# Kernel optimization log

Measured on AMD Instinct MI355X. Metric: run time of the kernel, lower is better.

## Reference

```python
import jax, jax.numpy as jnp
import numpy as np

N_NODES = 50000
N_EDGES = 800000
NODE_DIM = 128
HIDDEN = 256
LATENT = 128
COND = 5


def setup_inputs() -> dict:
    key = jax.random.key(0)
    ks = jax.random.split(key, 10)
    s = lambda d: 1.0 / np.sqrt(d)
    return {
        "node_features": jax.random.normal(ks[0], (N_NODES, NODE_DIM), jnp.float32),
        "conditions": jax.random.normal(ks[1], (COND,), jnp.float32),
        "src": jax.random.randint(ks[2], (N_EDGES,), 0, N_NODES, jnp.int32),
        "dst": jax.random.randint(ks[3], (N_EDGES,), 0, N_NODES, jnp.int32),
        "W1": jax.random.normal(ks[4], (NODE_DIM, HIDDEN), jnp.float32) * s(NODE_DIM),
        "b1": jnp.zeros((HIDDEN,), jnp.float32),
        "W2": jax.random.normal(ks[5], (HIDDEN, HIDDEN), jnp.float32) * s(HIDDEN),
        "b2": jnp.zeros((HIDDEN,), jnp.float32),
        "Wfc": jax.random.normal(ks[6], (HIDDEN + COND, LATENT), jnp.float32) * s(HIDDEN + COND),
        "bfc": jnp.zeros((LATENT,), jnp.float32),
        "Wmean": jax.random.normal(ks[7], (LATENT, LATENT), jnp.float32) * s(LATENT),
        "bmean": jnp.zeros((LATENT,), jnp.float32),
        "Wlogvar": jax.random.normal(ks[8], (LATENT, LATENT), jnp.float32) * s(LATENT),
        "blogvar": jnp.zeros((LATENT,), jnp.float32),
    }


def _graph_conv(x, src, dst, W, b, n_nodes):
    # gather source-node features along edges, sum-aggregate onto targets,
    # then linear transform: standard GraphConv (sum aggregation)
    agg = jax.ops.segment_sum(x[src], dst, num_segments=n_nodes)  # [N, d]
    return agg @ W + b


def reference(node_features, conditions, src, dst,
              W1, b1, W2, b2, Wfc, bfc, Wmean, bmean, Wlogvar, blogvar):
    n = node_features.shape[0]
    x = jax.nn.relu(_graph_conv(node_features, src, dst, W1, b1, n))  # [N, H]
    x = jax.nn.relu(_graph_conv(x, src, dst, W2, b2, n))              # [N, H]
    pooled = jnp.mean(x, axis=0)                                      # [H]
    h = jax.nn.relu(jnp.concatenate([pooled, conditions], axis=-1) @ Wfc + bfc)
    z_mean = h @ Wmean + bmean
    z_logvar = h @ Wlogvar + blogvar
    return z_mean, z_logvar
```

## Files before the change

### kernel.cpp

```cpp
#include <hip/hip_runtime.h>

#define N_NODES   50000
#define N_EDGES   800000
#define NODE_DIM  128
#define HIDDEN    256
#define LATENT    128
#define COND      5

#define NB        196
#define P1_CHUNK  4096
#define P1_GRID   ((N_EDGES + P1_CHUNK - 1) / P1_CHUNK)

typedef unsigned int uint;
typedef unsigned short ushort;
typedef unsigned char uchar;

typedef __attribute__((ext_vector_type(8))) short bf16x8;
typedef __attribute__((ext_vector_type(4))) float f32x4;

static __device__ __forceinline__ ushort f32_to_bf16(float f) {
    union { float f; uint u; } v; v.f = f;
    uint r = v.u + 0x7FFF + ((v.u >> 16) & 1);
    return (ushort)(r >> 16);
}
static __device__ __forceinline__ uint pack_bf16(float lo, float hi) {
    return (uint)f32_to_bf16(lo) | ((uint)f32_to_bf16(hi) << 16);
}

static __device__ __forceinline__ void gload_lds16(const void* g, void* l) {
    __builtin_amdgcn_global_load_lds(
        (const __attribute__((address_space(1))) unsigned int*)(unsigned long long)(uintptr_t)g,
        (__attribute__((address_space(3))) unsigned int*)(unsigned int)(uintptr_t)l,
        16, 0, 0);
}


#if __has_builtin(__builtin_amdgcn_cvt_pk_f32_fp8) && __has_builtin(__builtin_amdgcn_cvt_pk_fp8_f32)
#define HW_FP8 1
#endif

#ifndef HW_FP8
static __device__ __forceinline__ float dec1_fp8(uint b) {
    uint sgn = b & 0x80, mag = b & 0x7f;
    float v;
    if (mag >= 8) {
        union { uint u; float f; } t;
        t.u = (((mag >> 3) + 120) << 23) | ((mag & 7) << 20);
        v = t.f;
    } else {
        v = (float)mag * 0.001953125f;
    }
    return sgn ? -v : v;
}
static __device__ __forceinline__ uchar enc1_fp8(float f) {
    float a = fabsf(f);
    uint s = (f < 0.f) ? 0x80u : 0u;
    if (!(a >= 0.015625f)) {
        int q = (int)(a * 512.f + 0.5f);
        if (q > 7) q = 7;
        return (uchar)(s | (uint)q);
    }
    if (a >= 448.f) return (uchar)(s | 0x7E);
    union { float f; uint u; } t; t.f = a;
    uint e = (t.u >> 23) - 120;
    uint m = (t.u >> 20) & 7;
    uint rem = t.u & 0xFFFFF;
    uint v = (e << 3) | m;
    if (rem > 0x80000 || (rem == 0x80000 && (v & 1))) v++;
    if (v > 0x7E) v = 0x7E;
    return (uchar)(s | v);
}
#endif

static __device__ __forceinline__ void dec4_add(uint u, float* acc) {
#ifdef HW_FP8
    auto lo = __builtin_amdgcn_cvt_pk_f32_fp8((int)u, false);
    auto hi = __builtin_amdgcn_cvt_pk_f32_fp8((int)u, true);
    acc[0] += lo[0]; acc[1] += lo[1]; acc[2] += hi[0]; acc[3] += hi[1];
#else
    acc[0] += dec1_fp8(u & 0xff);
    acc[1] += dec1_fp8((u >> 8) & 0xff);
    acc[2] += dec1_fp8((u >> 16) & 0xff);
    acc[3] += dec1_fp8(u >> 24);
#endif
}
static __device__ __forceinline__ void dec2_add(uint u, float* acc) {
#ifdef HW_FP8
    auto lo = __builtin_amdgcn_cvt_pk_f32_fp8((int)u, false);
    acc[0] += lo[0]; acc[1] += lo[1];
#else
    acc[0] += dec1_fp8(u & 0xff);
    acc[1] += dec1_fp8((u >> 8) & 0xff);
#endif
}
static __device__ __forceinline__ uint enc2_fp8(float a, float b) {
#ifdef HW_FP8
    return (uint)__builtin_amdgcn_cvt_pk_fp8_f32(a, b, 0, false) & 0xFFFFu;
#else
    return (uint)enc1_fp8(a) | ((uint)enc1_fp8(b) << 8);
#endif
}
static __device__ __forceinline__ uchar enc1(float v) {
#ifdef HW_FP8
    return (uchar)(__builtin_amdgcn_cvt_pk_fp8_f32(v, v, 0, false) & 0xff);
#else
    return enc1_fp8(v);
#endif
}


#define NF4   (N_NODES * NODE_DIM / 4)
#define PREP1 (NF4 + NODE_DIM * HIDDEN)
#define PREP2 (PREP1 + HIDDEN * HIDDEN)
#define PREP3 (PREP2 + HIDDEN)
#define PREP4 (PREP3 + NB)
#define PREP5 (PREP4 + NB)
#define PREP6 (PREP5 + 1)

__global__ void prep_kernel(const float* __restrict__ nf,
                            const float* __restrict__ W1, const float* __restrict__ W2,
                            uchar* __restrict__ nf_fp8,
                            ushort* __restrict__ Wst1, ushort* __restrict__ Wst2,
                            float* __restrict__ pooled,
                            int* __restrict__ bcount, int* __restrict__ bcursor2,
                            int* __restrict__ hcnt) {
    int id = blockIdx.x * blockDim.x + threadIdx.x;
    if (id < NF4) {
        float4 v = reinterpret_cast<const float4*>(nf)[id];
        uint w = enc2_fp8(v.x, v.y) | (enc2_fp8(v.z, v.w) << 16);
        reinterpret_cast<uint*>(nf_fp8)[id] = w;
    } else if (id < PREP1) {
        int i = id - NF4;
        int k = i >> 8, c = i & 255;
        int idx = ((((k >> 5) * 16) + (((k & 31) >> 3) * 4 + (c >> 6))) * 64 + (c & 63)) * 8 + (k & 7);
        Wst1[idx] = f32_to_bf16(W1[i]);
    } else if (id < PREP2) {
        int i = id - PREP1;
        int k = i >> 8, c = i & 255;
        int idx = ((((k >> 5) * 16) + (((k & 31) >> 3) * 4 + (c >> 6))) * 64 + (c & 63)) * 8 + (k & 7);
        Wst2[idx] = f32_to_bf16(W2[i]);
    } else if (id < PREP3) {
        pooled[id - PREP2] = 0.f;
    } else if (id < PREP4) {
        bcount[id - PREP3] = 0;
    } else if (id < PREP5) {
        bcursor2[id - PREP4] = 0;
    } else if (id < PREP6) {
        hcnt[0] = 0;
    }
}


__global__ __launch_bounds__(256) void bcount_kernel(const int* __restrict__ dst,
                                                     int* __restrict__ bcount) {
    __shared__ int cnt[NB];
    const int t = threadIdx.x;
    for (int i = t; i < NB; i += 256) cnt[i] = 0;
    __syncthreads();
    const int base = blockIdx.x * P1_CHUNK;
#pragma unroll
    for (int i = 0; i < 16; ++i) {
        int e = base + i * 256 + t;
        if (e < N_EDGES) atomicAdd(&cnt[dst[e] >> 8], 1);
    }
    __syncthreads();
    for (int i = t; i < NB; i += 256)
        if (cnt[i] > 0) atomicAdd(&bcount[i], cnt[i]);
}

__global__ __launch_bounds__(256) void bwrite_kernel(const int* __restrict__ src,
                                                     const int* __restrict__ dst,
                                                     const int* __restrict__ bcount,
                                                     int* __restrict__ bcursor2,
                                                     uint* __restrict__ pair_buf) {
    __shared__ int s[256];
    __shared__ int cnt[NB];
    __shared__ int gbase[NB];
    const int t = threadIdx.x;
    s[t] = (t < NB) ? bcount[t] : 0;
    __syncthreads();
    for (int off = 1; off < 256; off <<= 1) {
        int v = (t >= off) ? s[t - off] : 0;
        __syncthreads();
        s[t] += v;
        __syncthreads();
    }
    for (int i = t; i < NB; i += 256) cnt[i] = 0;
    __syncthreads();

    const int base = blockIdx.x * P1_CHUNK;
    uint pk[16];
    int  bk[16], lr[16];
    bool ok[16];
#pragma unroll
    for (int i = 0; i < 16; ++i) {
        int e = base + i * 256 + t;
        ok[i] = e < N_EDGES;
        if (ok[i]) {
            int sv = src[e], d = dst[e];
            pk[i] = (uint)sv | ((uint)d << 16);
            bk[i] = d >> 8;
        }
    }
#pragma unroll
    for (int i = 0; i < 16; ++i)
        if (ok[i]) lr[i] = atomicAdd(&cnt[bk[i]], 1);
    __syncthreads();
    if (t < NB) {
        int c = cnt[t];
        if (c > 0) gbase[t] = ((t > 0) ? s[t - 1] : 0) + atomicAdd(&bcursor2[t], c);
    }
    __syncthreads();
#pragma unroll
    for (int i = 0; i < 16; ++i)
        if (ok[i]) pair_buf[gbase[bk[i]] + lr[i]] = pk[i];
}

__global__ __launch_bounds__(256) void csrloc_kernel(const uint* __restrict__ pair_buf,
                                                     const int* __restrict__ bcount,
                                                     int* __restrict__ offsets,
                                                     ushort* __restrict__ csr) {
    __shared__ int s[256];
    __shared__ int lcnt[256];
    __shared__ int loff[256];
    __shared__ int lcur[256];
    const int t = threadIdx.x;
    const int b = blockIdx.x;
    s[t] = (t < NB) ? bcount[t] : 0;
    __syncthreads();
    for (int off = 1; off < 256; off <<= 1) {
        int v = (t >= off) ? s[t - off] : 0;
        __syncthreads();
        s[t] += v;
        __syncthreads();
    }
    const int e0 = (b > 0) ? s[b - 1] : 0;
    const int e1 = s[b];
    lcnt[t] = 0;
    lcur[t] = 0;
    __syncthreads();

    for (int j = e0 + t; j < e1; j += 256)
        atomicAdd(&lcnt[(pair_buf[j] >> 16) & 255], 1);
    __syncthreads();

    const int myc = lcnt[t];
    s[t] = myc;
    __syncthreads();
    for (int off = 1; off < 256; off <<= 1) {
        int v = (t >= off) ? s[t - off] : 0;
        __syncthreads();
        s[t] += v;
        __syncthreads();
    }
    const int lofft = s[t] - myc;
    loff[t] = lofft;
    const int node = (b << 8) + t;
    if (node < N_NODES) offsets[node] = e0 + lofft;
    if (b == 0 && t == 0) offsets[N_NODES] = N_EDGES;
    __syncthreads();

    for (int j = e0 + t; j < e1; j += 256) {
        uint p = pair_buf[j];
        int dl = (int)(p >> 16) & 255;
        int r = atomicAdd(&lcur[dl], 1);
        csr[e0 + loff[dl] + r] = (ushort)(p & 0xFFFFu);
    }
}


template <int D>
__global__ __launch_bounds__(256) void agg_kernel(const uchar* __restrict__ x,
                                                  const int* __restrict__ offsets,
                                                  const ushort* __restrict__ csr,
                                                  ushort* __restrict__ out) {
    constexpr int BPL = D / 64;
    int node = (blockIdx.x * blockDim.x + threadIdx.x) >> 6;
    int lane = threadIdx.x & 63;
    if (node >= N_NODES) return;
    int j0 = __builtin_amdgcn_readfirstlane(offsets[node]);
    int j1 = __builtin_amdgcn_readfirstlane(offsets[node + 1]);

    float acc[BPL];
#pragma unroll
    for (int i = 0; i < BPL; ++i) acc[i] = 0.f;

    const uchar* base = x + lane * BPL;
    const int il = lane & 15;

    int idxv = (j0 + il < j1) ? (int)csr[j0 + il] : 0;

    for (int jb = j0; jb < j1; jb += 16) {
        int idxn = (jb + 16 + il < j1) ? (int)csr[jb + 16 + il] : 0;
        int n = j1 - jb; n = (n > 16) ? 16 : n;
        uint u[16];
        if (n == 16) {
#pragma unroll
            for (int i = 0; i < 16; ++i) {
                int s = __shfl(idxv, i);
                if constexpr (BPL == 4)
                    u[i] = *reinterpret_cast<const uint*>(base + (size_t)s * D);
                else
                    u[i] = *reinterpret_cast<const ushort*>(base + (size_t)s * D);
            }
#pragma unroll
            for (int i = 0; i < 16; ++i) {
                if constexpr (BPL == 4) dec4_add(u[i], acc); else dec2_add(u[i], acc);
            }
        } else {
#pragma unroll
            for (int i = 0; i < 16; ++i) {
                if (i < n) {
                    int s = __shfl(idxv, i);
                    if constexpr (BPL == 4)
                        u[i] = *reinterpret_cast<const uint*>(base + (size_t)s * D);
                    else
                        u[i] = *reinterpret_cast<const ushort*>(base + (size_t)s * D);
                }
            }
#pragma unroll
            for (int i = 0; i < 16; ++i) {
                if (i < n) {
                    if constexpr (BPL == 4) dec4_add(u[i], acc); else dec2_add(u[i], acc);
                }
            }
        }
        idxv = idxn;
    }

    if constexpr (BPL == 4) {
        uint2 o;
        o.x = pack_bf16(acc[0], acc[1]);
        o.y = pack_bf16(acc[2], acc[3]);
        *reinterpret_cast<uint2*>(out + (size_t)node * D + lane * 4) = o;
    } else {
        *reinterpret_cast<uint*>(out + (size_t)node * D + lane * 2) = pack_bf16(acc[0], acc[1]);
    }
}


__global__ __launch_bounds__(256) void gemm1_kernel(const ushort* __restrict__ A,
                                                    const ushort* __restrict__ Wst,
                                                    const float* __restrict__ bias,
                                                    uchar* __restrict__ Xout, int nblk) {
    constexpr int K = NODE_DIM;
    constexpr int NSTEP = K / 32;
    constexpr int WB    = NSTEP * 8 * 1024;
    constexpr int AB    = NSTEP * 4 * 1024;
    constexpr int NT    = (N_NODES + 63) / 64;
    __shared__ uchar lds[WB + 2 * AB];

    const int t    = threadIdx.x;
    const int lane = t & 63;
    const int wv   = t >> 6;
    const int fr   = lane & 15;
    const int kgl  = lane >> 4;
    const int half    = nblk >> 1;
    const int colhalf = blockIdx.x / half;
    const int stride  = half;

    const int kx = (lane & 3) ^ ((lane >> 3) & 3);

#pragma unroll
    for (int j = 0; j < NSTEP * 2; ++j) {
        const int lc = wv * (NSTEP * 2) + j;
        const int ks = lc >> 3, r = lc & 7;
        const int kg = r >> 1, ccl = r & 1;
        gload_lds16(Wst + ((size_t)ks * 16 + kg * 4 + colhalf * 2 + ccl) * 512 + lane * 8,
                    &lds[lc * 1024]);
    }

    auto stageA = [&](int buf, int row0) {
#pragma unroll
        for (int j = 0; j < NSTEP; ++j) {
            const int c  = wv * NSTEP + j;
            const int ks = c >> 2, rt = c & 3;
            gload_lds16(A + (size_t)(row0 + rt * 16 + (lane >> 2)) * K + ks * 32 + kx * 8,
                        &lds[WB + buf * AB + c * 1024]);
        }
    };

    const int rowsel = (wv & 1) * 2;
    const int colsel = wv >> 1;
    const int col0   = colhalf * 128 + colsel * 64;
    float bcol[4];
#pragma unroll
    for (int ct = 0; ct < 4; ++ct) bcol[ct] = bias[col0 + ct * 16 + fr];
    const int mrow = kgl * 4;
    const int aswz = (kgl ^ ((fr >> 1) & 3)) * 16;

    int tile = blockIdx.x % half;
    stageA(0, tile * 64);
    __syncthreads();

    for (int buf = 0; tile < NT; tile += stride, buf ^= 1) {
        const int tn = tile + stride;
        if (tn < NT) stageA(buf ^ 1, tn * 64);

        f32x4 acc[2][4];
#pragma unroll
        for (int rt = 0; rt < 2; ++rt)
#pragma unroll
            for (int ct = 0; ct < 4; ++ct)
                acc[rt][ct] = (f32x4){0.f, 0.f, 0.f, 0.f};

        const uchar* ab = &lds[WB + buf * AB];
#pragma unroll
        for (int ks = 0; ks < NSTEP; ++ks) {
            bf16x8 af[2], bfv[4];
#pragma unroll
            for (int rt = 0; rt < 2; ++rt)
                af[rt] = *reinterpret_cast<const bf16x8*>(ab + (ks * 4 + rowsel + rt) * 1024 + fr * 64 + aswz);
#pragma unroll
            for (int ct = 0; ct < 4; ++ct)
                bfv[ct] = *reinterpret_cast<const bf16x8*>(&lds[(ks * 8 + kgl * 2 + colsel) * 1024 + (ct * 16 + fr) * 16]);
#pragma unroll
            for (int rt = 0; rt < 2; ++rt)
#pragma unroll
                for (int ct = 0; ct < 4; ++ct)
                    acc[rt][ct] = __builtin_amdgcn_mfma_f32_16x16x32_bf16(af[rt], bfv[ct], acc[rt][ct], 0, 0, 0);
        }

        const int rowbase = tile * 64 + (wv & 1) * 32;
#pragma unroll
        for (int rt = 0; rt < 2; ++rt) {
#pragma unroll
            for (int e = 0; e < 4; ++e) {
                int m = rowbase + rt * 16 + mrow + e;
                if (m < N_NODES) {
#pragma unroll
                    for (int ct = 0; ct < 4; ++ct) {
                        float v = fmaxf(acc[rt][ct][e] + bcol[ct], 0.f);
                        Xout[(size_t)m * HIDDEN + col0 + ct * 16 + fr] = enc1(v);
                    }
                }
            }
        }
        __syncthreads();
    }
}


__global__ __launch_bounds__(256) void gemm2_kernel(const ushort* __restrict__ A,
                                                    const ushort* __restrict__ Wst,
                                                    const float* __restrict__ bias,
                                                    float* __restrict__ pooled, int nblk,
                                                    const float* __restrict__ cond,
                                                    const float* __restrict__ Wfc,
                                                    const float* __restrict__ bfc,
                                                    const float* __restrict__ Wmean,
                                                    const float* __restrict__ bmean,
                                                    const float* __restrict__ Wlogvar,
                                                    const float* __restrict__ blogvar,
                                                    float* __restrict__ outv,
                                                    int* __restrict__ hcnt) {
    constexpr int K   = HIDDEN;
    constexpr int WB  = 32768;
    constexpr int AB  = 16384;
    constexpr int NT  = (N_NODES + 31) / 32;
    __shared__ uchar lds[WB + 2 * AB];
    __shared__ int lastflag;

    const int t    = threadIdx.x;
    const int lane = t & 63;
    const int wv   = t >> 6;
    const int fr   = lane & 15;
    const int kgl  = lane >> 4;
    const int q      = nblk >> 2;
    const int colq   = blockIdx.x / q;
    const int stride = q;

    const int kx = (lane & 3) ^ ((lane >> 3) & 3);

#pragma unroll
    for (int j = 0; j < 8; ++j) {
        const int lc = wv * 8 + j;
        const int ks = lc >> 2, kg = lc & 3;
        gload_lds16(Wst + ((size_t)ks * 16 + kg * 4 + colq) * 512 + lane * 8,
                    &lds[lc * 1024]);
    }

    auto stageA = [&](int buf, int row0) {
#pragma unroll
        for (int j = 0; j < 4; ++j) {
            const int c  = wv * 4 + j;
            const int ks = c >> 1, rh = c & 1;
            gload_lds16(A + (size_t)(row0 + rh * 16 + (lane >> 2)) * K + ks * 32 + kx * 8,
                        &lds[WB + buf * AB + c * 1024]);
        }
    };

    const int rowhalf = wv & 1;
    const int colh32  = wv >> 1;
    const int col0    = colq * 64 + colh32 * 32;
    float bcol[2];
#pragma unroll
    for (int ct = 0; ct < 2; ++ct) bcol[ct] = bias[col0 + ct * 16 + fr];
    const int mrow = kgl * 4;
    const int aswz = (kgl ^ ((fr >> 1) & 3)) * 16;

    float cs[2] = {0.f, 0.f};
    int tile = blockIdx.x % q;
    stageA(0, tile * 32);
    __syncthreads();

    for (int buf = 0; tile < NT; tile += stride, buf ^= 1) {
        const int tn = tile + stride;
        if (tn < NT) stageA(buf ^ 1, tn * 32);

        f32x4 acc[2];
        acc[0] = (f32x4){0.f, 0.f, 0.f, 0.f};
        acc[1] = (f32x4){0.f, 0.f, 0.f, 0.f};

        const uchar* ab = &lds[WB + buf * AB];
#pragma unroll
        for (int ks = 0; ks < 8; ++ks) {
            bf16x8 af, bfv[2];
            af = *reinterpret_cast<const bf16x8*>(ab + (ks * 2 + rowhalf) * 1024 + fr * 64 + aswz);
#pragma unroll
            for (int ct = 0; ct < 2; ++ct)
                bfv[ct] = *reinterpret_cast<const bf16x8*>(
                    &lds[(ks * 4 + kgl) * 1024 + (colh32 * 32 + ct * 16 + fr) * 16]);
#pragma unroll
            for (int ct = 0; ct < 2; ++ct)
                acc[ct] = __builtin_amdgcn_mfma_f32_16x16x32_bf16(af, bfv[ct], acc[ct], 0, 0, 0);
        }

        const int rowbase = tile * 32 + rowhalf * 16;
#pragma unroll
        for (int e = 0; e < 4; ++e) {
            int m = rowbase + mrow + e;
            if (m < N_NODES) {
                cs[0] += fmaxf(acc[0][e] + bcol[0], 0.f);
                cs[1] += fmaxf(acc[1][e] + bcol[1], 0.f);
            }
        }
        __syncthreads();
    }

#pragma unroll
    for (int ct = 0; ct < 2; ++ct) {
        cs[ct] += __shfl_xor(cs[ct], 16);
        cs[ct] += __shfl_xor(cs[ct], 32);
    }
    if (lane < 16) {
#pragma unroll
        for (int ct = 0; ct < 2; ++ct)
            atomicAdd(&pooled[col0 + ct * 16 + lane], cs[ct]);
    }

    asm volatile("s_waitcnt vmcnt(0)" ::: "memory");
    __syncthreads();
    if (t == 0) lastflag = (atomicAdd(hcnt, 1) == nblk - 1) ? 1 : 0;
    __syncthreads();
    if (lastflag) {
        float* hv = (float*)lds;
        float* hh = (float*)(lds + 2048);
        if (t < HIDDEN) hv[t] = atomicAdd(&pooled[t], 0.0f) * (1.0f / N_NODES);
        if (t < COND) hv[HIDDEN + t] = cond[t];
        __syncthreads();
        if (t < LATENT) {
            float s = bfc[t];
            for (int k = 0; k < HIDDEN + COND; ++k) s += hv[k] * Wfc[k * LATENT + t];
            hh[t] = fmaxf(s, 0.f);
        }
        __syncthreads();
        if (t < LATENT) {
            float s = bmean[t];
            for (int k = 0; k < LATENT; ++k) s += hh[k] * Wmean[k * LATENT + t];
            outv[t] = s;
        } else if (t < 2 * LATENT) {
            int j = t - LATENT;
            float s = blogvar[j];
            for (int k = 0; k < LATENT; ++k) s += hh[k] * Wlogvar[k * LATENT + j];
            outv[LATENT + j] = s;
        }
    }
}


extern "C" void kernel_launch(void* const* d_in, const int* in_sizes, int n_in,
                              void* d_out, int out_size, void* d_ws, size_t ws_size,
                              hipStream_t stream) {
    const float* node_features = (const float*)d_in[0];
    const float* conditions    = (const float*)d_in[1];
    const int*   src           = (const int*)d_in[2];
    const int*   dst           = (const int*)d_in[3];
    const float* W1  = (const float*)d_in[4];
    const float* b1  = (const float*)d_in[5];
    const float* W2  = (const float*)d_in[6];
    const float* b2  = (const float*)d_in[7];
    const float* Wfc = (const float*)d_in[8];
    const float* bfc = (const float*)d_in[9];
    const float* Wmean   = (const float*)d_in[10];
    const float* bmean   = (const float*)d_in[11];
    const float* Wlogvar = (const float*)d_in[12];
    const float* blogvar = (const float*)d_in[13];
    float* out = (float*)d_out;

    size_t o = 0;
    auto alloc = [&](size_t bytes) {
        void* p = (char*)d_ws + o;
        o += (bytes + 255) & ~(size_t)255;
        return p;
    };
    int* offsets   = (int*)alloc((size_t)(N_NODES + 1) * 4);
    int* bcount    = (int*)alloc((size_t)NB * 4);
    int* bcursor2  = (int*)alloc((size_t)NB * 4);
    int* hcnt      = (int*)alloc(4);
    uint* pair_buf = (uint*)alloc((size_t)N_EDGES * 4);
    ushort* csr    = (ushort*)alloc((size_t)N_EDGES * 2);
    float* pooled  = (float*)alloc(HIDDEN * 4);
    ushort* Wst1   = (ushort*)alloc((size_t)HIDDEN * NODE_DIM * 2);
    ushort* Wst2   = (ushort*)alloc((size_t)HIDDEN * HIDDEN * 2);
    uchar* nf_fp8  = (uchar*)alloc((size_t)N_NODES * NODE_DIM);
    uchar* x1_fp8  = (uchar*)alloc((size_t)N_NODES * HIDDEN);
    ushort* agg1   = (ushort*)alloc((size_t)(N_NODES + 64) * NODE_DIM * 2);
    ushort* agg2   = (ushort*)alloc((size_t)(N_NODES + 64) * HIDDEN * 2);

    prep_kernel<<<(PREP6 + 255) / 256, 256, 0, stream>>>(
        node_features, W1, W2, nf_fp8, Wst1, Wst2, pooled, bcount, bcursor2, hcnt);

    bcount_kernel<<<P1_GRID, 256, 0, stream>>>(dst, bcount);
    bwrite_kernel<<<P1_GRID, 256, 0, stream>>>(src, dst, bcount, bcursor2, pair_buf);
    csrloc_kernel<<<NB, 256, 0, stream>>>(pair_buf, bcount, offsets, csr);

    const int AGG_GRID = (N_NODES * 64 + 255) / 256;
    const int G1_BLK = 512;
    const int G2_BLK = 512;

    agg_kernel<NODE_DIM><<<AGG_GRID, 256, 0, stream>>>(nf_fp8, offsets, csr, agg1);
    gemm1_kernel<<<G1_BLK, 256, 0, stream>>>(agg1, Wst1, b1, x1_fp8, G1_BLK);

    agg_kernel<HIDDEN><<<AGG_GRID, 256, 0, stream>>>(x1_fp8, offsets, csr, agg2);
    gemm2_kernel<<<G2_BLK, 256, 0, stream>>>(
        agg2, Wst2, b2, pooled, G2_BLK,
        conditions, Wfc, bfc, Wmean, bmean, Wlogvar, blogvar, out, hcnt);
}
```

Baseline: 141.2 us.

## Load GEMM operands directly into registers instead of staging through LDS

Both GEMM kernels drop the LDS double-buffered staging with global_load_lds and instead load weight fragments once into registers and A fragments per tile directly from global memory. The weight pre-layout becomes a plain transpose (column-major bf16), and barriers inside the tile loop are removed. This is meant to cut LDS traffic and synchronisation overhead, but it loses explicit prefetch overlap and raises register pressure (launch_bounds 256,2 added), with less coalesced global reads of A.

```diff
diff --git a/kernel.cpp b/kernel.cpp
--- a/kernel.cpp
+++ b/kernel.cpp
@@ -25,13 +25,6 @@
 }
 static __device__ __forceinline__ uint pack_bf16(float lo, float hi) {
     return (uint)f32_to_bf16(lo) | ((uint)f32_to_bf16(hi) << 16);
-}
-
-static __device__ __forceinline__ void gload_lds16(const void* g, void* l) {
-    __builtin_amdgcn_global_load_lds(
-        (const __attribute__((address_space(1))) unsigned int*)(unsigned long long)(uintptr_t)g,
-        (__attribute__((address_space(3))) unsigned int*)(unsigned int)(uintptr_t)l,
-        16, 0, 0);
 }
 
 
@@ -120,7 +113,7 @@
 __global__ void prep_kernel(const float* __restrict__ nf,
                             const float* __restrict__ W1, const float* __restrict__ W2,
                             uchar* __restrict__ nf_fp8,
-                            ushort* __restrict__ Wst1, ushort* __restrict__ Wst2,
+                            ushort* __restrict__ Wt1, ushort* __restrict__ Wt2,
                             float* __restrict__ pooled,
                             int* __restrict__ bcount, int* __restrict__ bcursor2,
                             int* __restrict__ hcnt) {
@@ -132,13 +125,11 @@
     } else if (id < PREP1) {
         int i = id - NF4;
         int k = i >> 8, c = i & 255;
-        int idx = ((((k >> 5) * 16) + (((k & 31) >> 3) * 4 + (c >> 6))) * 64 + (c & 63)) * 8 + (k & 7);
-        Wst1[idx] = f32_to_bf16(W1[i]);
+        Wt1[c * NODE_DIM + k] = f32_to_bf16(W1[i]);
     } else if (id < PREP2) {
         int i = id - PREP1;
         int k = i >> 8, c = i & 255;
-        int idx = ((((k >> 5) * 16) + (((k & 31) >> 3) * 4 + (c >> 6))) * 64 + (c & 63)) * 8 + (k & 7);
-        Wst2[idx] = f32_to_bf16(W2[i]);
+        Wt2[c * HIDDEN + k] = f32_to_bf16(W2[i]);
     } else if (id < PREP3) {
         pooled[id - PREP2] = 0.f;
     } else if (id < PREP4) {
@@ -339,63 +330,48 @@
 }
 
 
-__global__ __launch_bounds__(256) void gemm1_kernel(const ushort* __restrict__ A,
-                                                    const ushort* __restrict__ Wst,
-                                                    const float* __restrict__ bias,
-                                                    uchar* __restrict__ Xout, int nblk) {
-    constexpr int K = NODE_DIM;
-    constexpr int NSTEP = K / 32;
-    constexpr int WB    = NSTEP * 8 * 1024;
-    constexpr int AB    = NSTEP * 4 * 1024;
-    constexpr int NT    = (N_NODES + 63) / 64;
-    __shared__ uchar lds[WB + 2 * AB];
-
-    const int t    = threadIdx.x;
-    const int lane = t & 63;
-    const int wv   = t >> 6;
+__global__ __launch_bounds__(256, 2) void gemm1_kernel(const ushort* __restrict__ A,
+                                                       const ushort* __restrict__ Wt,
+                                                       const float* __restrict__ bias,
+                                                       uchar* __restrict__ Xout, int nblk) {
+    constexpr int K  = NODE_DIM;
+    constexpr int NT = (N_NODES + 63) / 64;
+
+    const int lane = threadIdx.x & 63;
+    const int wv   = threadIdx.x >> 6;
     const int fr   = lane & 15;
     const int kgl  = lane >> 4;
     const int half    = nblk >> 1;
     const int colhalf = blockIdx.x / half;
     const int stride  = half;
 
-    const int kx = (lane & 3) ^ ((lane >> 3) & 3);
-
-#pragma unroll
-    for (int j = 0; j < NSTEP * 2; ++j) {
-        const int lc = wv * (NSTEP * 2) + j;
-        const int ks = lc >> 3, r = lc & 7;
-        const int kg = r >> 1, ccl = r & 1;
-        gload_lds16(Wst + ((size_t)ks * 16 + kg * 4 + colhalf * 2 + ccl) * 512 + lane * 8,
-                    &lds[lc * 1024]);
-    }
-
-    auto stageA = [&](int buf, int row0) {
-#pragma unroll
-        for (int j = 0; j < NSTEP; ++j) {
-            const int c  = wv * NSTEP + j;
-            const int ks = c >> 2, rt = c & 3;
-            gload_lds16(A + (size_t)(row0 + rt * 16 + (lane >> 2)) * K + ks * 32 + kx * 8,
-                        &lds[WB + buf * AB + c * 1024]);
-        }
-    };
-
-    const int rowsel = (wv & 1) * 2;
+    const int rowsel = (wv & 1) * 32;
     const int colsel = wv >> 1;
     const int col0   = colhalf * 128 + colsel * 64;
+
+    bf16x8 w[4][4];
+#pragma unroll
+    for (int ks = 0; ks < 4; ++ks)
+#pragma unroll
+        for (int ct = 0; ct < 4; ++ct)
+            w[ks][ct] = *reinterpret_cast<const bf16x8*>(
+                Wt + (size_t)(col0 + ct * 16 + fr) * K + ks * 32 + kgl * 8);
+
     float bcol[4];
 #pragma unroll
     for (int ct = 0; ct < 4; ++ct) bcol[ct] = bias[col0 + ct * 16 + fr];
     const int mrow = kgl * 4;
-    const int aswz = (kgl ^ ((fr >> 1) & 3)) * 16;
-
-    int tile = blockIdx.x % half;
-    stageA(0, tile * 64);
-    __syncthreads();
-
-    for (int buf = 0; tile < NT; tile += stride, buf ^= 1) {
-        const int tn = tile + stride;
-        if (tn < NT) stageA(buf ^ 1, tn * 64);
+
+    for (int tile = blockIdx.x % half; tile < NT; tile += stride) {
+        const int rowb = tile * 64 + rowsel;
+        bf16x8 af[2][4];
+#pragma unroll
+        for (int rt = 0; rt < 2; ++rt) {
+            const ushort* ap = A + (size_t)(rowb + rt * 16 + fr) * K + kgl * 8;
+#pragma unroll
+            for (int ks = 0; ks < 4; ++ks)
+                af[rt][ks] = *reinterpret_cast<const bf16x8*>(ap + ks * 32);
+        }
 
         f32x4 acc[2][4];
 #pragma unroll
@@ -404,29 +380,19 @@
             for (int ct = 0; ct < 4; ++ct)
                 acc[rt][ct] = (f32x4){0.f, 0.f, 0.f, 0.f};
 
-        const uchar* ab = &lds[WB + buf * AB];
-#pragma unroll
-        for (int ks = 0; ks < NSTEP; ++ks) {
-            bf16x8 af[2], bfv[4];
+#pragma unroll
+        for (int ks = 0; ks < 4; ++ks)
 #pragma unroll
             for (int rt = 0; rt < 2; ++rt)
-                af[rt] = *reinterpret_cast<const bf16x8*>(ab + (ks * 4 + rowsel + rt) * 1024 + fr * 64 + aswz);
-#pragma unroll
-            for (int ct = 0; ct < 4; ++ct)
-                bfv[ct] = *reinterpret_cast<const bf16x8*>(&lds[(ks * 8 + kgl * 2 + colsel) * 1024 + (ct * 16 + fr) * 16]);
-#pragma unroll
-            for (int rt = 0; rt < 2; ++rt)
 #pragma unroll
                 for (int ct = 0; ct < 4; ++ct)
-                    acc[rt][ct] = __builtin_amdgcn_mfma_f32_16x16x32_bf16(af[rt], bfv[ct], acc[rt][ct], 0, 0, 0);
-        }
-
-        const int rowbase = tile * 64 + (wv & 1) * 32;
+                    acc[rt][ct] = __builtin_amdgcn_mfma_f32_16x16x32_bf16(af[rt][ks], w[ks][ct], acc[rt][ct], 0, 0, 0);
+
 #pragma unroll
         for (int rt = 0; rt < 2; ++rt) {
 #pragma unroll
             for (int e = 0; e < 4; ++e) {
-                int m = rowbase + rt * 16 + mrow + e;
+                int m = rowb + rt * 16 + mrow + e;
                 if (m < N_NODES) {
 #pragma unroll
                     for (int ct = 0; ct < 4; ++ct) {
@@ -436,29 +402,27 @@
                 }
             }
         }
-        __syncthreads();
-    }
-}
-
-
-__global__ __launch_bounds__(256) void gemm2_kernel(const ushort* __restrict__ A,
-                                                    const ushort* __restrict__ Wst,
-                                                    const float* __restrict__ bias,
-                                                    float* __restrict__ pooled, int nblk,
-                                                    const float* __restrict__ cond,
-                                                    const float* __restrict__ Wfc,
-                                                    const float* __restrict__ bfc,
-                                                    const float* __restrict__ Wmean,
-                                                    const float* __restrict__ bmean,
-                                                    const float* __restrict__ Wlogvar,
-                                                    const float* __restrict__ blogvar,
-                                                    float* __restrict__ outv,
-                                                    int* __restrict__ hcnt) {
-    constexpr int K   = HIDDEN;
-    constexpr int WB  = 32768;
-    constexpr int AB  = 16384;
-    constexpr int NT  = (N_NODES + 31) / 32;
-    __shared__ uchar lds[WB + 2 * AB];
+    }
+}
+
+
+__global__ __launch_bounds__(256, 2) void gemm2_kernel(const ushort* __restrict__ A,
+                                                       const ushort* __restrict__ Wt,
+                                                       const float* __restrict__ bias,
+                                                       float* __restrict__ pooled, int nblk,
+                                                       const float* __restrict__ cond,
+                                                       const float* __restrict__ Wfc,
+                                                       const float* __restrict__ bfc,
+                                                       const float* __restrict__ Wmean,
+                                                       const float* __restrict__ bmean,
+                                                       const float* __restrict__ Wlogvar,
+                                                       const float* __restrict__ blogvar,
+                                                       float* __restrict__ outv,
+                                                       int* __restrict__ hcnt) {
+    constexpr int K  = HIDDEN;
+    constexpr int NT = (N_NODES + 31) / 32;
+    __shared__ float hv[HIDDEN + COND];
+    __shared__ float hh[LATENT];
     __shared__ int lastflag;
 
     const int t    = threadIdx.x;
@@ -470,72 +434,50 @@
     const int colq   = blockIdx.x / q;
     const int stride = q;
 
-    const int kx = (lane & 3) ^ ((lane >> 3) & 3);
-
-#pragma unroll
-    for (int j = 0; j < 8; ++j) {
-        const int lc = wv * 8 + j;
-        const int ks = lc >> 2, kg = lc & 3;
-        gload_lds16(Wst + ((size_t)ks * 16 + kg * 4 + colq) * 512 + lane * 8,
-                    &lds[lc * 1024]);
-    }
-
-    auto stageA = [&](int buf, int row0) {
-#pragma unroll
-        for (int j = 0; j < 4; ++j) {
-            const int c  = wv * 4 + j;
-            const int ks = c >> 1, rh = c & 1;
-            gload_lds16(A + (size_t)(row0 + rh * 16 + (lane >> 2)) * K + ks * 32 + kx * 8,
-                        &lds[WB + buf * AB + c * 1024]);
-        }
-    };
-
     const int rowhalf = wv & 1;
     const int colh32  = wv >> 1;
     const int col0    = colq * 64 + colh32 * 32;
+
+    bf16x8 w[8][2];
+#pragma unroll
+    for (int ks = 0; ks < 8; ++ks)
+#pragma unroll
+        for (int ct = 0; ct < 2; ++ct)
+            w[ks][ct] = *reinterpret_cast<const bf16x8*>(
+                Wt + (size_t)(col0 + ct * 16 + fr) * K + ks * 32 + kgl * 8);
+
     float bcol[2];
-#pragma unroll
-    for (int ct = 0; ct < 2; ++ct) bcol[ct] = bias[col0 + ct * 16 + fr];
+    bcol[0] = bias[col0 + fr];
+    bcol[1] = bias[col0 + 16 + fr];
     const int mrow = kgl * 4;
-    const int aswz = (kgl ^ ((fr >> 1) & 3)) * 16;
 
     float cs[2] = {0.f, 0.f};
-    int tile = blockIdx.x % q;
-    stageA(0, tile * 32);
-    __syncthreads();
-
-    for (int buf = 0; tile < NT; tile += stride, buf ^= 1) {
-        const int tn = tile + stride;
-        if (tn < NT) stageA(buf ^ 1, tn * 32);
+
+    for (int tile = blockIdx.x % q; tile < NT; tile += stride) {
+        const int rowb = tile * 32 + rowhalf * 16;
+        const ushort* ap = A + (size_t)(rowb + fr) * K + kgl * 8;
+        bf16x8 af[8];
+#pragma unroll
+        for (int ks = 0; ks < 8; ++ks)
+            af[ks] = *reinterpret_cast<const bf16x8*>(ap + ks * 32);
 
         f32x4 acc[2];
         acc[0] = (f32x4){0.f, 0.f, 0.f, 0.f};
         acc[1] = (f32x4){0.f, 0.f, 0.f, 0.f};
-
-        const uchar* ab = &lds[WB + buf * AB];
 #pragma unroll
         for (int ks = 0; ks < 8; ++ks) {
-            bf16x8 af, bfv[2];
-            af = *reinterpret_cast<const bf16x8*>(ab + (ks * 2 + rowhalf) * 1024 + fr * 64 + aswz);
-#pragma unroll
-            for (int ct = 0; ct < 2; ++ct)
-                bfv[ct] = *reinterpret_cast<const bf16x8*>(
-                    &lds[(ks * 4 + kgl) * 1024 + (colh32 * 32 + ct * 16 + fr) * 16]);
-#pragma unroll
-            for (int ct = 0; ct < 2; ++ct)
-                acc[ct] = __builtin_amdgcn_mfma_f32_16x16x32_bf16(af, bfv[ct], acc[ct], 0, 0, 0);
-        }
-
-        const int rowbase = tile * 32 + rowhalf * 16;
+            acc[0] = __builtin_amdgcn_mfma_f32_16x16x32_bf16(af[ks], w[ks][0], acc[0], 0, 0, 0);
+            acc[1] = __builtin_amdgcn_mfma_f32_16x16x32_bf16(af[ks], w[ks][1], acc[1], 0, 0, 0);
+        }
+
 #pragma unroll
         for (int e = 0; e < 4; ++e) {
-            int m = rowbase + mrow + e;
+            int m = rowb + mrow + e;
             if (m < N_NODES) {
                 cs[0] += fmaxf(acc[0][e] + bcol[0], 0.f);
                 cs[1] += fmaxf(acc[1][e] + bcol[1], 0.f);
             }
         }
-        __syncthreads();
     }
 
 #pragma unroll
@@ -554,8 +496,6 @@
     if (t == 0) lastflag = (atomicAdd(hcnt, 1) == nblk - 1) ? 1 : 0;
     __syncthreads();
     if (lastflag) {
-        float* hv = (float*)lds;
-        float* hh = (float*)(lds + 2048);
         if (t < HIDDEN) hv[t] = atomicAdd(&pooled[t], 0.0f) * (1.0f / N_NODES);
         if (t < COND) hv[HIDDEN + t] = cond[t];
         __syncthreads();
@@ -611,15 +551,15 @@
     uint* pair_buf = (uint*)alloc((size_t)N_EDGES * 4);
     ushort* csr    = (ushort*)alloc((size_t)N_EDGES * 2);
     float* pooled  = (float*)alloc(HIDDEN * 4);
-    ushort* Wst1   = (ushort*)alloc((size_t)HIDDEN * NODE_DIM * 2);
-    ushort* Wst2   = (ushort*)alloc((size_t)HIDDEN * HIDDEN * 2);
+    ushort* Wt1    = (ushort*)alloc((size_t)HIDDEN * NODE_DIM * 2);
+    ushort* Wt2    = (ushort*)alloc((size_t)HIDDEN * HIDDEN * 2);
     uchar* nf_fp8  = (uchar*)alloc((size_t)N_NODES * NODE_DIM);
     uchar* x1_fp8  = (uchar*)alloc((size_t)N_NODES * HIDDEN);
     ushort* agg1   = (ushort*)alloc((size_t)(N_NODES + 64) * NODE_DIM * 2);
     ushort* agg2   = (ushort*)alloc((size_t)(N_NODES + 64) * HIDDEN * 2);
 
     prep_kernel<<<(PREP6 + 255) / 256, 256, 0, stream>>>(
-        node_features, W1, W2, nf_fp8, Wst1, Wst2, pooled, bcount, bcursor2, hcnt);
+        node_features, W1, W2, nf_fp8, Wt1, Wt2, pooled, bcount, bcursor2, hcnt);
 
     bcount_kernel<<<P1_GRID, 256, 0, stream>>>(dst, bcount);
     bwrite_kernel<<<P1_GRID, 256, 0, stream>>>(src, dst, bcount, bcursor2, pair_buf);
@@ -630,10 +570,10 @@
     const int G2_BLK = 512;
 
     agg_kernel<NODE_DIM><<<AGG_GRID, 256, 0, stream>>>(nf_fp8, offsets, csr, agg1);
-    gemm1_kernel<<<G1_BLK, 256, 0, stream>>>(agg1, Wst1, b1, x1_fp8, G1_BLK);
+    gemm1_kernel<<<G1_BLK, 256, 0, stream>>>(agg1, Wt1, b1, x1_fp8, G1_BLK);
 
     agg_kernel<HIDDEN><<<AGG_GRID, 256, 0, stream>>>(x1_fp8, offsets, csr, agg2);
     gemm2_kernel<<<G2_BLK, 256, 0, stream>>>(
-        agg2, Wst2, b2, pooled, G2_BLK,
+        agg2, Wt2, b2, pooled, G2_BLK,
         conditions, Wfc, bfc, Wmean, bmean, Wlogvar, blogvar, out, hcnt);
 }
```

Result: slower. 163.3 us (+15.6%).
